# Optimization experiments

Measured on AMD Instinct MI355X. Metric: run time of the kernel, lower is better.

The kernel has to match this reference:

```python
import jax, jax.numpy as jnp
import numpy as np

N_NODES = 100000
N_EDGES = 500000
NODE_DIM = 128
EDGE_DIM = 64
HIDDEN = 128
IN_DIM = 2 * NODE_DIM + EDGE_DIM  # 320
EPS = 1e-5


def _layer_norm(h, g, b):
    mu = jnp.mean(h, axis=-1, keepdims=True)
    var = jnp.var(h, axis=-1, keepdims=True)
    return (h - mu) * jax.lax.rsqrt(var + EPS) * g + b


def setup_inputs() -> dict:
    key = jax.random.key(0)
    ks = jax.random.split(key, 12)
    sc_in = 1.0 / np.sqrt(IN_DIM)
    sc_h = 1.0 / np.sqrt(HIDDEN)
    sc_e = 1.0 / np.sqrt(EDGE_DIM)
    return {
        "x": jax.random.normal(ks[0], (N_NODES, NODE_DIM), jnp.float32),
        "edge_index": jax.random.randint(ks[1], (2, N_EDGES), 0, N_NODES, jnp.int32),
        "edge_attr": jax.random.normal(ks[2], (N_EDGES, EDGE_DIM), jnp.float32),
        "W1": jax.random.uniform(ks[3], (IN_DIM, HIDDEN), jnp.float32, -sc_in, sc_in),
        "b1": jnp.zeros((HIDDEN,), jnp.float32),
        "g1": jnp.ones((HIDDEN,), jnp.float32),
        "be1": jnp.zeros((HIDDEN,), jnp.float32),
        "W2": jax.random.uniform(ks[4], (HIDDEN, HIDDEN), jnp.float32, -sc_h, sc_h),
        "b2": jnp.zeros((HIDDEN,), jnp.float32),
        "Wg": jax.random.uniform(ks[5], (IN_DIM, HIDDEN), jnp.float32, -sc_in, sc_in),
        "bg": jnp.zeros((HIDDEN,), jnp.float32),
        "Wr": jax.random.uniform(ks[6], (EDGE_DIM, HIDDEN), jnp.float32, -sc_e, sc_e),
        "br": jnp.zeros((HIDDEN,), jnp.float32),
        "g2": jnp.ones((HIDDEN,), jnp.float32),
        "be2": jnp.zeros((HIDDEN,), jnp.float32),
    }


def reference(x, edge_index, edge_attr, W1, b1, g1, be1, W2, b2, Wg, bg, Wr, br, g2, be2):
    src, dst = edge_index[0], edge_index[1]
    # [E, 2*node_dim + edge_dim]
    cat_feat = jnp.concatenate([x[src], x[dst], edge_attr], axis=-1)
    # mlp: Linear -> LayerNorm -> GELU(exact) -> (dropout=id) -> Linear
    h = _layer_norm(cat_feat @ W1 + b1, g1, be1)
    h = jax.nn.gelu(h, approximate=False)
    update = h @ W2 + b2
    gate = jax.nn.sigmoid(cat_feat @ Wg + bg)
    res = edge_attr @ Wr + br  # res_proj (edge_dim != hidden_dim)
    return _layer_norm(update * gate + res, g2, be2)
```

## Files before the change

### kernel.cpp

```cpp
#include <hip/hip_runtime.h>
#include <hip/hip_bf16.h>
#include <math.h>

typedef __attribute__((ext_vector_type(8))) short short8;
typedef __attribute__((ext_vector_type(4))) float f32x4;

namespace {
constexpr int E_TOTAL = 500000;
constexpr int ND  = 128;
constexpr int ED  = 64;
constexpr int KIN = 320;
constexpr int H   = 128;
constexpr int ME  = 64;
constexpr int RS  = 328;
constexpr float EPS = 1e-5f;
constexpr int OFF_W1T = 0;
constexpr int OFF_WGT = 40960;
constexpr int OFF_W2T = 81920;
constexpr int OFF_WRT = 98304;
}

__device__ __forceinline__ unsigned short f2bf(float f) {
  union { __hip_bfloat16 h; unsigned short u; } cv;
  cv.h = __float2bfloat16(f);
  return cv.u;
}
__device__ __forceinline__ unsigned pack2(float a, float b) {
  return (unsigned)f2bf(a) | ((unsigned)f2bf(b) << 16);
}

__global__ void prep_weights(const float* __restrict__ W1, const float* __restrict__ Wg,
                             const float* __restrict__ W2, const float* __restrict__ Wr,
                             short* __restrict__ wt) {
  const int t = blockIdx.x * 256 + threadIdx.x;
  if (t < 40960) {
    const int n = t / KIN, k = t % KIN;
    wt[OFF_W1T + t] = (short)f2bf(W1[k * H + n]);
    wt[OFF_WGT + t] = (short)f2bf(Wg[k * H + n]);
  }
  if (t < 16384) {
    const int n = t / H, k = t % H;
    wt[OFF_W2T + t] = (short)f2bf(W2[k * H + n]);
  }
  if (t < 8192) {
    const int n = t / ED, k = t % ED;
    wt[OFF_WRT + t] = (short)f2bf(Wr[k * H + n]);
  }
}

__global__ __launch_bounds__(256, 2) void edge_mfma_kernel(
    const float* __restrict__ x, const int* __restrict__ ei, const float* __restrict__ ea,
    const short* __restrict__ wt,
    const float* __restrict__ b1, const float* __restrict__ g1, const float* __restrict__ be1,
    const float* __restrict__ b2, const float* __restrict__ bg, const float* __restrict__ br,
    const float* __restrict__ g2, const float* __restrict__ be2,
    float* __restrict__ out)
{
  __shared__ short catA[ME * RS];
  __shared__ float red[ME][8];
  __shared__ int   sidx[ME], didx[ME];

  const int t    = threadIdx.x;
  const int w    = t >> 6;
  const int lane = t & 63;
  const int g    = lane >> 4;
  const int l15  = lane & 15;
  const long e0  = (long)blockIdx.x * ME;

  if (t < ME) {
    long eg = e0 + t; if (eg >= E_TOTAL) eg = E_TOTAL - 1;
    sidx[t] = ei[eg];
  } else if (t < 2 * ME) {
    long eg = e0 + (t - ME); if (eg >= E_TOTAL) eg = E_TOTAL - 1;
    didx[t - ME] = ei[E_TOTAL + eg];
  }
  __syncthreads();

  {
    const int c = lane << 1;
    for (int i = 0; i < 16; ++i) {
      const int e = i * 4 + w;
      const float2 xs = *(const float2*)(x + (long)sidx[e] * ND + c);
      const float2 xd = *(const float2*)(x + (long)didx[e] * ND + c);
      *(unsigned*)&catA[e * RS + c]      = pack2(xs.x, xs.y);
      *(unsigned*)&catA[e * RS + ND + c] = pack2(xd.x, xd.y);
    }
    const int e8 = t >> 5;
    const int c2 = (t & 31) << 1;
    for (int i = 0; i < 8; ++i) {
      const int e = i * 8 + e8;
      long eg = e0 + e; if (eg >= E_TOTAL) eg = E_TOTAL - 1;
      const float2 v = *(const float2*)(ea + eg * ED + c2);
      *(unsigned*)&catA[e * RS + 2 * ND + c2] = pack2(v.x, v.y);
    }
  }
  __syncthreads();

  const int col0 = w * 32 + l15;
  const int col1 = w * 32 + 16 + l15;

  f32x4 accH[4][2], accG[4][2];
  {
    const float bh0 = b1[col0], bh1 = b1[col1];
    const float bg0 = bg[col0], bg1 = bg[col1];
    #pragma unroll
    for (int mt = 0; mt < 4; ++mt) {
      accH[mt][0] = (f32x4){bh0, bh0, bh0, bh0};
      accH[mt][1] = (f32x4){bh1, bh1, bh1, bh1};
      accG[mt][0] = (f32x4){bg0, bg0, bg0, bg0};
      accG[mt][1] = (f32x4){bg1, bg1, bg1, bg1};
    }
  }
  {
    const short* pW1a = wt + OFF_W1T + col0 * KIN + g * 8;
    const short* pW1b = wt + OFF_W1T + col1 * KIN + g * 8;
    const short* pWga = wt + OFF_WGT + col0 * KIN + g * 8;
    const short* pWgb = wt + OFF_WGT + col1 * KIN + g * 8;
    for (int ks = 0; ks < KIN / 32; ++ks) {
      const int ko = ks * 32 + g * 8;
      short8 a[4];
      #pragma unroll
      for (int mt = 0; mt < 4; ++mt)
        a[mt] = *(const short8*)&catA[(mt * 16 + l15) * RS + ko];
      const short8 bW1a = *(const short8*)(pW1a + ks * 32);
      const short8 bW1b = *(const short8*)(pW1b + ks * 32);
      const short8 bWga = *(const short8*)(pWga + ks * 32);
      const short8 bWgb = *(const short8*)(pWgb + ks * 32);
      #pragma unroll
      for (int mt = 0; mt < 4; ++mt) {
        accH[mt][0] = __builtin_amdgcn_mfma_f32_16x16x32_bf16(a[mt], bW1a, accH[mt][0], 0, 0, 0);
        accH[mt][1] = __builtin_amdgcn_mfma_f32_16x16x32_bf16(a[mt], bW1b, accH[mt][1], 0, 0, 0);
        accG[mt][0] = __builtin_amdgcn_mfma_f32_16x16x32_bf16(a[mt], bWga, accG[mt][0], 0, 0, 0);
        accG[mt][1] = __builtin_amdgcn_mfma_f32_16x16x32_bf16(a[mt], bWgb, accG[mt][1], 0, 0, 0);
      }
    }
  }

  #pragma unroll
  for (int mt = 0; mt < 4; ++mt) {
    f32x4 ps = accH[mt][0] + accH[mt][1];
    f32x4 pq = accH[mt][0] * accH[mt][0] + accH[mt][1] * accH[mt][1];
    #pragma unroll
    for (int off = 1; off < 16; off <<= 1) {
      #pragma unroll
      for (int r = 0; r < 4; ++r) {
        ps[r] += __shfl_xor(ps[r], off);
        pq[r] += __shfl_xor(pq[r], off);
      }
    }
    if (l15 == 0) {
      #pragma unroll
      for (int r = 0; r < 4; ++r) {
        red[mt * 16 + g * 4 + r][w * 2]     = ps[r];
        red[mt * 16 + g * 4 + r][w * 2 + 1] = pq[r];
      }
    }
  }
  __syncthreads();

  {
    const float g1v0 = g1[col0], g1v1 = g1[col1];
    const float be10 = be1[col0], be11 = be1[col1];
    #pragma unroll
    for (int mt = 0; mt < 4; ++mt) {
      #pragma unroll
      for (int r = 0; r < 4; ++r) {
        const int row = mt * 16 + g * 4 + r;
        const float4 ra = *(const float4*)&red[row][0];
        const float4 rb = *(const float4*)&red[row][4];
        const float sum = ra.x + ra.z + rb.x + rb.z;
        const float sq  = ra.y + ra.w + rb.y + rb.w;
        const float m   = sum * (1.0f / H);
        float var = sq * (1.0f / H) - m * m;
        var = fmaxf(var, 0.0f);
        const float rs = rsqrtf(var + EPS);
        float h0 = (accH[mt][0][r] - m) * rs * g1v0 + be10;
        float h1 = (accH[mt][1][r] - m) * rs * g1v1 + be11;
        h0 = h0 * 0.5f * (1.0f + erff(h0 * 0.70710678118654752f));
        h1 = h1 * 0.5f * (1.0f + erff(h1 * 0.70710678118654752f));
        catA[row * RS + col0] = (short)f2bf(h0);
        catA[row * RS + col1] = (short)f2bf(h1);
        accG[mt][0][r] = 1.0f / (1.0f + __expf(-accG[mt][0][r]));
        accG[mt][1][r] = 1.0f / (1.0f + __expf(-accG[mt][1][r]));
      }
    }
  }
  __syncthreads();

  f32x4 accU[4][2], accR[4][2];
  {
    const float bu0 = b2[col0], bu1 = b2[col1];
    const float br0 = br[col0], br1 = br[col1];
    #pragma unroll
    for (int mt = 0; mt < 4; ++mt) {
      accU[mt][0] = (f32x4){bu0, bu0, bu0, bu0};
      accU[mt][1] = (f32x4){bu1, bu1, bu1, bu1};
      accR[mt][0] = (f32x4){br0, br0, br0, br0};
      accR[mt][1] = (f32x4){br1, br1, br1, br1};
    }
  }
  {
    const short* pW2a = wt + OFF_W2T + col0 * H + g * 8;
    const short* pW2b = wt + OFF_W2T + col1 * H + g * 8;
    for (int ks = 0; ks < H / 32; ++ks) {
      const int ko = ks * 32 + g * 8;
      short8 a[4];
      #pragma unroll
      for (int mt = 0; mt < 4; ++mt)
        a[mt] = *(const short8*)&catA[(mt * 16 + l15) * RS + ko];
      const short8 b0 = *(const short8*)(pW2a + ks * 32);
      const short8 b1v = *(const short8*)(pW2b + ks * 32);
      #pragma unroll
      for (int mt = 0; mt < 4; ++mt) {
        accU[mt][0] = __builtin_amdgcn_mfma_f32_16x16x32_bf16(a[mt], b0, accU[mt][0], 0, 0, 0);
        accU[mt][1] = __builtin_amdgcn_mfma_f32_16x16x32_bf16(a[mt], b1v, accU[mt][1], 0, 0, 0);
      }
    }
    const short* pWra = wt + OFF_WRT + col0 * ED + g * 8;
    const short* pWrb = wt + OFF_WRT + col1 * ED + g * 8;
    for (int ks = 0; ks < ED / 32; ++ks) {
      const int ko = 2 * ND + ks * 32 + g * 8;
      short8 a[4];
      #pragma unroll
      for (int mt = 0; mt < 4; ++mt)
        a[mt] = *(const short8*)&catA[(mt * 16 + l15) * RS + ko];
      const short8 b0 = *(const short8*)(pWra + ks * 32);
      const short8 b1v = *(const short8*)(pWrb + ks * 32);
      #pragma unroll
      for (int mt = 0; mt < 4; ++mt) {
        accR[mt][0] = __builtin_amdgcn_mfma_f32_16x16x32_bf16(a[mt], b0, accR[mt][0], 0, 0, 0);
        accR[mt][1] = __builtin_amdgcn_mfma_f32_16x16x32_bf16(a[mt], b1v, accR[mt][1], 0, 0, 0);
      }
    }
  }

  #pragma unroll
  for (int mt = 0; mt < 4; ++mt) {
    accU[mt][0] = accU[mt][0] * accG[mt][0] + accR[mt][0];
    accU[mt][1] = accU[mt][1] * accG[mt][1] + accR[mt][1];
  }

  #pragma unroll
  for (int mt = 0; mt < 4; ++mt) {
    f32x4 ps = accU[mt][0] + accU[mt][1];
    f32x4 pq = accU[mt][0] * accU[mt][0] + accU[mt][1] * accU[mt][1];
    #pragma unroll
    for (int off = 1; off < 16; off <<= 1) {
      #pragma unroll
      for (int r = 0; r < 4; ++r) {
        ps[r] += __shfl_xor(ps[r], off);
        pq[r] += __shfl_xor(pq[r], off);
      }
    }
    if (l15 == 0) {
      #pragma unroll
      for (int r = 0; r < 4; ++r) {
        red[mt * 16 + g * 4 + r][w * 2]     = ps[r];
        red[mt * 16 + g * 4 + r][w * 2 + 1] = pq[r];
      }
    }
  }
  __syncthreads();
  {
    const float g2v0 = g2[col0], g2v1 = g2[col1];
    const float be20 = be2[col0], be21 = be2[col1];
    #pragma unroll
    for (int mt = 0; mt < 4; ++mt) {
      #pragma unroll
      for (int r = 0; r < 4; ++r) {
        const int row = mt * 16 + g * 4 + r;
        const float4 ra = *(const float4*)&red[row][0];
        const float4 rb = *(const float4*)&red[row][4];
        const float sum = ra.x + ra.z + rb.x + rb.z;
        const float sq  = ra.y + ra.w + rb.y + rb.w;
        const float m   = sum * (1.0f / H);
        float var = sq * (1.0f / H) - m * m;
        var = fmaxf(var, 0.0f);
        const float rs = rsqrtf(var + EPS);
        const long eg = e0 + row;
        if (eg < E_TOTAL) {
          out[eg * H + col0] = (accU[mt][0][r] - m) * rs * g2v0 + be20;
          out[eg * H + col1] = (accU[mt][1][r] - m) * rs * g2v1 + be21;
        }
      }
    }
  }
}

extern "C" void kernel_launch(void* const* d_in, const int* in_sizes, int n_in,
                              void* d_out, int out_size, void* d_ws, size_t ws_size,
                              hipStream_t stream) {
  const float* x   = (const float*)d_in[0];
  const int*   ei  = (const int*)  d_in[1];
  const float* ea  = (const float*)d_in[2];
  const float* W1  = (const float*)d_in[3];
  const float* b1  = (const float*)d_in[4];
  const float* g1  = (const float*)d_in[5];
  const float* be1 = (const float*)d_in[6];
  const float* W2  = (const float*)d_in[7];
  const float* b2  = (const float*)d_in[8];
  const float* Wg  = (const float*)d_in[9];
  const float* bg  = (const float*)d_in[10];
  const float* Wr  = (const float*)d_in[11];
  const float* br  = (const float*)d_in[12];
  const float* g2  = (const float*)d_in[13];
  const float* be2 = (const float*)d_in[14];
  float* out = (float*)d_out;
  short* wt  = (short*)d_ws;

  prep_weights<<<160, 256, 0, stream>>>(W1, Wg, W2, Wr, wt);

  const int grid = (E_TOTAL + ME - 1) / ME;
  edge_mfma_kernel<<<grid, 256, 0, stream>>>(
      x, ei, ea, wt, b1, g1, be1, b2, bg, br, g2, be2, out);
}
```

Before: 642.8 us.

## Read edge_attr fragments directly from global, shrink LDS row, raise occupancy, fast GELU

Stops staging edge_attr into shared memory and instead builds bf16 MFMA A-fragments straight from global memory for both the first GEMM's tail and the residual projection. The shared row stride drops from 328 to 264, which cuts LDS per block, and launch bounds are raised to 4 blocks per CU to increase occupancy. Exact erf is replaced with an Abramowitz-Stegun polynomial, and rcp/rsq intrinsics are used for the sigmoid and layer-norm scaling. The trade-offs are that edge_attr is read from global memory twice, register pressure may rise or spill under the tighter launch bound, and the erf approximation adds small numerical error.

```diff
diff --git a/kernel.cpp b/kernel.cpp
--- a/kernel.cpp
+++ b/kernel.cpp
@@ -12,7 +12,7 @@
 constexpr int KIN = 320;
 constexpr int H   = 128;
 constexpr int ME  = 64;
-constexpr int RS  = 328;
+constexpr int RS  = 264;
 constexpr float EPS = 1e-5f;
 constexpr int OFF_W1T = 0;
 constexpr int OFF_WGT = 40960;
@@ -27,6 +27,32 @@
 }
 __device__ __forceinline__ unsigned pack2(float a, float b) {
   return (unsigned)f2bf(a) | ((unsigned)f2bf(b) << 16);
+}
+
+__device__ __forceinline__ float gelu_erf(float x) {
+  const float s = x * 0.70710678118654752f;
+  const float a = fabsf(s);
+  const float t = __builtin_amdgcn_rcpf(fmaf(0.3275911f, a, 1.0f));
+  float p = fmaf(1.061405429f, t, -1.453152027f);
+  p = fmaf(p, t, 1.421413741f);
+  p = fmaf(p, t, -0.284496736f);
+  p = fmaf(p, t, 0.254829592f);
+  p = p * t;
+  const float e = __expf(-a * a);
+  float er = fmaf(-p, e, 1.0f);
+  er = copysignf(er, s);
+  return 0.5f * x * (1.0f + er);
+}
+
+__device__ __forceinline__ short8 ea_frag(const float* __restrict__ er, int kk) {
+  const float4 f0 = *(const float4*)(er + kk);
+  const float4 f1 = *(const float4*)(er + kk + 4);
+  union { short8 s; unsigned u[4]; } cv;
+  cv.u[0] = pack2(f0.x, f0.y);
+  cv.u[1] = pack2(f0.z, f0.w);
+  cv.u[2] = pack2(f1.x, f1.y);
+  cv.u[3] = pack2(f1.z, f1.w);
+  return cv.s;
 }
 
 __global__ void prep_weights(const float* __restrict__ W1, const float* __restrict__ Wg,
@@ -48,7 +74,7 @@
   }
 }
 
-__global__ __launch_bounds__(256, 2) void edge_mfma_kernel(
+__global__ __launch_bounds__(256, 4) void edge_mfma_kernel(
     const float* __restrict__ x, const int* __restrict__ ei, const float* __restrict__ ea,
     const short* __restrict__ wt,
     const float* __restrict__ b1, const float* __restrict__ g1, const float* __restrict__ be1,
@@ -85,14 +111,13 @@
       *(unsigned*)&catA[e * RS + c]      = pack2(xs.x, xs.y);
       *(unsigned*)&catA[e * RS + ND + c] = pack2(xd.x, xd.y);
     }
-    const int e8 = t >> 5;
-    const int c2 = (t & 31) << 1;
-    for (int i = 0; i < 8; ++i) {
-      const int e = i * 8 + e8;
-      long eg = e0 + e; if (eg >= E_TOTAL) eg = E_TOTAL - 1;
-      const float2 v = *(const float2*)(ea + eg * ED + c2);
-      *(unsigned*)&catA[e * RS + 2 * ND + c2] = pack2(v.x, v.y);
-    }
+  }
+
+  const float* eaR[4];
+  #pragma unroll
+  for (int mt = 0; mt < 4; ++mt) {
+    long eg = e0 + mt * 16 + l15; if (eg >= E_TOTAL) eg = E_TOTAL - 1;
+    eaR[mt] = ea + eg * (long)ED;
   }
   __syncthreads();
 
@@ -116,7 +141,7 @@
     const short* pW1b = wt + OFF_W1T + col1 * KIN + g * 8;
     const short* pWga = wt + OFF_WGT + col0 * KIN + g * 8;
     const short* pWgb = wt + OFF_WGT + col1 * KIN + g * 8;
-    for (int ks = 0; ks < KIN / 32; ++ks) {
+    for (int ks = 0; ks < 8; ++ks) {
       const int ko = ks * 32 + g * 8;
       short8 a[4];
       #pragma unroll
@@ -132,6 +157,22 @@
         accH[mt][1] = __builtin_amdgcn_mfma_f32_16x16x32_bf16(a[mt], bW1b, accH[mt][1], 0, 0, 0);
         accG[mt][0] = __builtin_amdgcn_mfma_f32_16x16x32_bf16(a[mt], bWga, accG[mt][0], 0, 0, 0);
         accG[mt][1] = __builtin_amdgcn_mfma_f32_16x16x32_bf16(a[mt], bWgb, accG[mt][1], 0, 0, 0);
+      }
+    }
+    #pragma unroll
+    for (int ks = 0; ks < 2; ++ks) {
+      const int kk = ks * 32 + g * 8;
+      const short8 bW1a = *(const short8*)(pW1a + (8 + ks) * 32);
+      const short8 bW1b = *(const short8*)(pW1b + (8 + ks) * 32);
+      const short8 bWga = *(const short8*)(pWga + (8 + ks) * 32);
+      const short8 bWgb = *(const short8*)(pWgb + (8 + ks) * 32);
+      #pragma unroll
+      for (int mt = 0; mt < 4; ++mt) {
+        const short8 am = ea_frag(eaR[mt], kk);
+        accH[mt][0] = __builtin_amdgcn_mfma_f32_16x16x32_bf16(am, bW1a, accH[mt][0], 0, 0, 0);
+        accH[mt][1] = __builtin_amdgcn_mfma_f32_16x16x32_bf16(am, bW1b, accH[mt][1], 0, 0, 0);
+        accG[mt][0] = __builtin_amdgcn_mfma_f32_16x16x32_bf16(am, bWga, accG[mt][0], 0, 0, 0);
+        accG[mt][1] = __builtin_amdgcn_mfma_f32_16x16x32_bf16(am, bWgb, accG[mt][1], 0, 0, 0);
       }
     }
   }
@@ -173,15 +214,15 @@
         const float m   = sum * (1.0f / H);
         float var = sq * (1.0f / H) - m * m;
         var = fmaxf(var, 0.0f);
-        const float rs = rsqrtf(var + EPS);
+        const float rs = __builtin_amdgcn_rsqf(var + EPS);
         float h0 = (accH[mt][0][r] - m) * rs * g1v0 + be10;
         float h1 = (accH[mt][1][r] - m) * rs * g1v1 + be11;
-        h0 = h0 * 0.5f * (1.0f + erff(h0 * 0.70710678118654752f));
-        h1 = h1 * 0.5f * (1.0f + erff(h1 * 0.70710678118654752f));
+        h0 = gelu_erf(h0);
+        h1 = gelu_erf(h1);
         catA[row * RS + col0] = (short)f2bf(h0);
         catA[row * RS + col1] = (short)f2bf(h1);
-        accG[mt][0][r] = 1.0f / (1.0f + __expf(-accG[mt][0][r]));
-        accG[mt][1][r] = 1.0f / (1.0f + __expf(-accG[mt][1][r]));
+        accG[mt][0][r] = __builtin_amdgcn_rcpf(1.0f + __expf(-accG[mt][0][r]));
+        accG[mt][1][r] = __builtin_amdgcn_rcpf(1.0f + __expf(-accG[mt][1][r]));
       }
     }
   }
@@ -218,18 +259,16 @@
     }
     const short* pWra = wt + OFF_WRT + col0 * ED + g * 8;
     const short* pWrb = wt + OFF_WRT + col1 * ED + g * 8;
-    for (int ks = 0; ks < ED / 32; ++ks) {
-      const int ko = 2 * ND + ks * 32 + g * 8;
-      short8 a[4];
-      #pragma unroll
-      for (int mt = 0; mt < 4; ++mt)
-        a[mt] = *(const short8*)&catA[(mt * 16 + l15) * RS + ko];
+    #pragma unroll
+    for (int ks = 0; ks < 2; ++ks) {
+      const int kk = ks * 32 + g * 8;
       const short8 b0 = *(const short8*)(pWra + ks * 32);
       const short8 b1v = *(const short8*)(pWrb + ks * 32);
       #pragma unroll
       for (int mt = 0; mt < 4; ++mt) {
-        accR[mt][0] = __builtin_amdgcn_mfma_f32_16x16x32_bf16(a[mt], b0, accR[mt][0], 0, 0, 0);
-        accR[mt][1] = __builtin_amdgcn_mfma_f32_16x16x32_bf16(a[mt], b1v, accR[mt][1], 0, 0, 0);
+        const short8 am = ea_frag(eaR[mt], kk);
+        accR[mt][0] = __builtin_amdgcn_mfma_f32_16x16x32_bf16(am, b0, accR[mt][0], 0, 0, 0);
+        accR[mt][1] = __builtin_amdgcn_mfma_f32_16x16x32_bf16(am, b1v, accR[mt][1], 0, 0, 0);
       }
     }
   }
@@ -276,7 +315,7 @@
         const float m   = sum * (1.0f / H);
         float var = sq * (1.0f / H) - m * m;
         var = fmaxf(var, 0.0f);
-        const float rs = rsqrtf(var + EPS);
+        const float rs = __builtin_amdgcn_rsqf(var + EPS);
         const long eg = e0 + row;
         if (eg < E_TOTAL) {
           out[eg * H + col0] = (accU[mt][0][r] - m) * rs * g2v0 + be20;
```

New measurement: 744.3 us. 15.8% more time.
